# Kernel tuning notes

Hardware: AMD Instinct MI355X
Metric: run time of the kernel (lower is better)

Reference implementation:

```python
import jax, jax.numpy as jnp
import numpy as np

H, W, C, KH, KW = 16, 16, 3, 3, 3  # SOMLayer(16,16,3,3,3)
STRIDE = 2


def _extract_patches(x):
    """x: [B,C,Himg,Wimg] -> patches [B, P, C*KH*KW] in (C,kh,kw) order, P = n_out^2."""
    n_out = (x.shape[-2] - KH) // STRIDE + 1  # 15 for 32x32 input
    starts = jnp.arange(n_out) * STRIDE
    rows = starts[:, None] + jnp.arange(KH)   # [n_out, KH]
    cols = starts[:, None] + jnp.arange(KW)   # [n_out, KW]
    xr = x[:, :, rows, :]                      # [B,C,n_out,KH,Wimg]
    xrc = xr[:, :, :, :, cols]                 # [B,C,n_out,KH,n_out,KW]
    p = jnp.transpose(xrc, (0, 2, 4, 1, 3, 5)) # [B,n_out,n_out,C,KH,KW]
    return p.reshape(x.shape[0], n_out * n_out, C * KH * KW), n_out


def _som_forward(x, som):
    """Batched cdist+argmin over all windows and all 256 codebook cells.
    Faithful to the torch nested loops: winner = argmin_{m,n} mean((patch - som[m,n])^2),
    flat index m*W+n, first-occurrence tie-break (matches torch.min).
    argmin is invariant to the /27 mean scaling, so we use squared-distance GEMM form."""
    p, n_out = _extract_patches(x)             # [B,P,27]
    s = som.reshape(H * W, -1)                 # [256,27]
    d = ((p * p).sum(-1)[:, :, None]
         + (s * s).sum(-1)[None, None, :]
         - 2.0 * jnp.einsum('bpk,ck->bpc', p, s))  # [B,P,256]
    win = jnp.argmin(d, axis=-1)               # [B,P]
    m = (win // W).astype(jnp.float32) / H     # winner_r / som.shape[0]
    n = (win % W).astype(jnp.float32) / W      # winner_c / som.shape[1]
    B = x.shape[0]
    return jnp.stack([m, n], axis=1).reshape(B, 2, n_out, n_out)  # [B,2,15,15]


def setup_inputs() -> dict:
    key = jax.random.key(0)
    ks = jax.random.split(key, 10)
    B = 2048
    x = jax.random.uniform(ks[0], (B, 3, 32, 32), dtype=jnp.float32)
    # codebook (torch inits to constant 0.5 which degenerates argmin to all-ties;
    # we use a trained-like random codebook in [0,1])
    som = jax.random.uniform(ks[1], (H, W, C, KH, KW), dtype=jnp.float32)
    def lin(k, fo, fi):
        kw, kb = jax.random.split(k)
        s = 1.0 / np.sqrt(fi)
        return (jax.random.uniform(kw, (fo, fi), jnp.float32, -s, s),
                jax.random.uniform(kb, (fo,), jnp.float32, -s, s))
    W1, b1 = lin(ks[2], 400, 2 * 15 * 15)
    W2, b2 = lin(ks[3], 200, 400)
    W3, b3 = lin(ks[4], 100, 200)
    W4, b4 = lin(ks[5], 10, 100)
    return {"x": x, "som": som, "W1": W1, "b1": b1, "W2": W2, "b2": b2,
            "W3": W3, "b3": b3, "W4": W4, "b4": b4, "som_coef": 0}


def reference(x, som, W1, b1, W2, b2, W3, b3, W4, b4, som_coef):
    # som_coef=0 (and with the default momentum=1.0 the EMA update is a no-op anyway),
    # so the SOM pass is the pure winner-lookup; output is detached in torch -> stop_gradient.
    feat = jax.lax.stop_gradient(_som_forward(x, som))  # [B,2,15,15]
    h = feat.reshape(x.shape[0], -1)                    # [B,450]
    h = jax.nn.relu(h @ W1.T + b1)   # dropout in eval mode = identity
    h = jax.nn.relu(h @ W2.T + b2)
    h = jax.nn.relu(h @ W3.T + b3)
    return h @ W4.T + b4             # [B,10]
```

## Files before the change

kernel.cpp:

```cpp
#include <hip/hip_runtime.h>
#include <hip/hip_bf16.h>

#define NOUT    15
#define NPATCH  225
#define BATCH   2048
#define FEATDIM 450
#define NPTOT   (BATCH * NPATCH)
#define SOMBYTES 49152

typedef __attribute__((ext_vector_type(4))) float f32x4;
typedef __attribute__((ext_vector_type(2))) float f32x2;
typedef __attribute__((ext_vector_type(8))) short bf16x8s;

static __device__ __forceinline__ short bf2s(__hip_bfloat16 h) {
    union { __hip_bfloat16 b; short s; } u; u.b = h; return u.s;
}

__global__ void prep_som(const float* __restrict__ som, short* __restrict__ sbuf) {
    int c = threadIdx.x;
    int ct = c >> 4, col = c & 15;
    float s2 = 0.f;
    #pragma unroll
    for (int k = 0; k < 27; ++k) { float v = som[c * 27 + k]; s2 = fmaf(v, v, s2); }
    float bias = -0.5f * s2;
    #pragma unroll
    for (int kc = 0; kc < 4; ++kc)
        #pragma unroll
        for (int j = 0; j < 8; ++j) {
            int k = kc * 8 + j;
            float v = (k < 27) ? som[c * 27 + k] : ((k == 27) ? bias : 0.f);
            __hip_bfloat16 h = __float2bfloat16(v);
            float r1 = v - __bfloat162float(h);
            __hip_bfloat16 m = __float2bfloat16(r1);
            float r2 = r1 - __bfloat162float(m);
            int base = (ct * 192 + kc * 16 + col) * 8 + j;
            sbuf[base]        = bf2s(h);
            sbuf[base + 512]  = bf2s(m);
            sbuf[base + 1024] = bf2s(__float2bfloat16(r2));
        }
}

__global__ __launch_bounds__(1024, 4) void som_mfma(const float* __restrict__ x,
                                                    const short* __restrict__ sbuf,
                                                    float* __restrict__ feat) {
    __shared__ short SB[SOMBYTES / 2];

    const int tid = threadIdx.x;
    {
        const uint4* g = (const uint4*)sbuf;
        uint4* l = (uint4*)SB;
        #pragma unroll
        for (int i = 0; i < 3; ++i) l[tid + i * 1024] = g[tid + i * 1024];
    }

    const int wv   = tid >> 6;
    const int lane = tid & 63;
    const int row  = lane & 15;
    const int kc   = lane >> 4;
    const int col  = lane & 15;

    bf16x8s ah[2], am[2], al[2];
    #pragma unroll
    for (int s = 0; s < 2; ++s) {
        unsigned gp = blockIdx.x * 512u + wv * 32u + s * 16u + row;
        unsigned b  = gp / 225u;
        unsigned t  = gp - b * 225u;
        unsigned oi = t / 15u, oj = t - oi * 15u;
        const float* xb = x + (size_t)b * 3072 + oi * 64 + oj * 2;
        #pragma unroll
        for (int j = 0; j < 8; ++j) {
            int k = kc * 8 + j;
            float v = 0.f;
            if (k < 27) {
                int c = k / 9, rr = k - c * 9;
                int kh = rr / 3, kw = rr - kh * 3;
                v = xb[c * 1024 + kh * 32 + kw];
            } else if (k == 27) {
                v = 1.0f;
            }
            __hip_bfloat16 h = __float2bfloat16(v);
            float r1 = v - __bfloat162float(h);
            __hip_bfloat16 mm = __float2bfloat16(r1);
            float r2 = r1 - __bfloat162float(mm);
            ah[s][j] = bf2s(h);
            am[s][j] = bf2s(mm);
            al[s][j] = bf2s(__float2bfloat16(r2));
        }
    }
    __syncthreads();

    const bf16x8s* SBC = (const bf16x8s*)SB;

    f32x4 best[2];
    int   bidx[2][4];
    #pragma unroll
    for (int s = 0; s < 2; ++s) {
        best[s] = (f32x4){-1e30f, -1e30f, -1e30f, -1e30f};
        #pragma unroll
        for (int i = 0; i < 4; ++i) bidx[s][i] = 0;
    }

    #pragma unroll
    for (int ct = 0; ct < 16; ++ct) {
        bf16x8s bh = SBC[ct * 192 + lane];
        bf16x8s bm = SBC[ct * 192 + 64 + lane];
        bf16x8s bl = SBC[ct * 192 + 128 + lane];
        #pragma unroll
        for (int s = 0; s < 2; ++s) {
            f32x4 accA = {0.f, 0.f, 0.f, 0.f};
            f32x4 accB = {0.f, 0.f, 0.f, 0.f};
            accA = __builtin_amdgcn_mfma_f32_16x16x32_bf16(al[s], bh, accA, 0, 0, 0);
            accB = __builtin_amdgcn_mfma_f32_16x16x32_bf16(ah[s], bl, accB, 0, 0, 0);
            accA = __builtin_amdgcn_mfma_f32_16x16x32_bf16(am[s], bm, accA, 0, 0, 0);
            accB = __builtin_amdgcn_mfma_f32_16x16x32_bf16(am[s], bh, accB, 0, 0, 0);
            accA = __builtin_amdgcn_mfma_f32_16x16x32_bf16(ah[s], bm, accA, 0, 0, 0);
            accB = __builtin_amdgcn_mfma_f32_16x16x32_bf16(ah[s], bh, accB, 0, 0, 0);
            #pragma unroll
            for (int i = 0; i < 4; ++i) {
                float sc = accA[i] + accB[i];
                bool g = sc > best[s][i];
                best[s][i] = g ? sc : best[s][i];
                bidx[s][i] = g ? (ct * 16 + col) : bidx[s][i];
            }
        }
    }

    #pragma unroll
    for (int m = 1; m < 16; m <<= 1) {
        #pragma unroll
        for (int s = 0; s < 2; ++s)
            #pragma unroll
            for (int i = 0; i < 4; ++i) {
                float ob = __shfl_xor(best[s][i], m, 64);
                int   oi2 = __shfl_xor(bidx[s][i], m, 64);
                if (ob > best[s][i] || (ob == best[s][i] && oi2 < bidx[s][i])) {
                    best[s][i] = ob; bidx[s][i] = oi2;
                }
            }
    }

    if (col == 0) {
        #pragma unroll
        for (int s = 0; s < 2; ++s)
            #pragma unroll
            for (int i = 0; i < 4; ++i) {
                unsigned gp2 = blockIdx.x * 512u + wv * 32u + s * 16u + kc * 4u + i;
                unsigned b2  = gp2 / 225u;
                unsigned t2  = gp2 - b2 * 225u;
                feat[(size_t)b2 * FEATDIM + t2]          = (float)(bidx[s][i] >> 4) * 0.0625f;
                feat[(size_t)b2 * FEATDIM + NPATCH + t2] = (float)(bidx[s][i] & 15) * 0.0625f;
            }
    }
}

template <int RELU>
__global__ __launch_bounds__(128) void mlp_gemm(const float* __restrict__ A,
                                                const float* __restrict__ Wt,
                                                const float* __restrict__ bias,
                                                float* __restrict__ out,
                                                int M, int N, int K) {
    __shared__ float As[32][34];
    __shared__ float Bs[32][66];

    const int tid = threadIdx.x;
    const int m0 = blockIdx.y * 32;
    const int n0 = blockIdx.x * 64;
    const int tn = tid & 15, tm = tid >> 4;
    const int mA = tid & 31, ko = tid >> 5;
    const int nB = tid & 63, kh = tid >> 6;

    const f32x2 z2 = {0.f, 0.f};
    f32x2 pa[4], pb[8];
    float acc[4][4];
    #pragma unroll
    for (int i = 0; i < 4; ++i)
        #pragma unroll
        for (int j = 0; j < 4; ++j) acc[i][j] = 0.f;

    const bool nOk = (n0 + nB) < N;
    const int iters = (K + 31) / 32;

    #pragma unroll
    for (int q = 0; q < 4; ++q) {
        int k = ko * 8 + 2 * q;
        pa[q] = (k < K) ? *(const f32x2*)&A[(size_t)(m0 + mA) * K + k] : z2;
    }
    #pragma unroll
    for (int q = 0; q < 8; ++q) {
        int k = kh * 16 + 2 * q;
        pb[q] = (k < K && nOk) ? *(const f32x2*)&Wt[(size_t)(n0 + nB) * K + k] : z2;
    }

    for (int it = 0; it < iters; ++it) {
        #pragma unroll
        for (int q = 0; q < 4; ++q) {
            As[ko * 8 + 2 * q][mA]     = pa[q].x;
            As[ko * 8 + 2 * q + 1][mA] = pa[q].y;
        }
        #pragma unroll
        for (int q = 0; q < 8; ++q) {
            Bs[kh * 16 + 2 * q][nB]     = pb[q].x;
            Bs[kh * 16 + 2 * q + 1][nB] = pb[q].y;
        }
        __syncthreads();

        if (it + 1 < iters) {
            int kb = (it + 1) * 32;
            #pragma unroll
            for (int q = 0; q < 4; ++q) {
                int k = kb + ko * 8 + 2 * q;
                pa[q] = (k < K) ? *(const f32x2*)&A[(size_t)(m0 + mA) * K + k] : z2;
            }
            #pragma unroll
            for (int q = 0; q < 8; ++q) {
                int k = kb + kh * 16 + 2 * q;
                pb[q] = (k < K && nOk) ? *(const f32x2*)&Wt[(size_t)(n0 + nB) * K + k] : z2;
            }
        }

        #pragma unroll
        for (int k = 0; k < 32; ++k) {
            f32x4 a4 = *(const f32x4*)&As[k][tm * 4];
            f32x4 b4 = *(const f32x4*)&Bs[k][tn * 4];
            #pragma unroll
            for (int i = 0; i < 4; ++i)
                #pragma unroll
                for (int j = 0; j < 4; ++j)
                    acc[i][j] = fmaf(a4[i], b4[j], acc[i][j]);
        }
        __syncthreads();
    }

    #pragma unroll
    for (int i = 0; i < 4; ++i) {
        int m = m0 + tm * 4 + i;
        #pragma unroll
        for (int j = 0; j < 4; ++j) {
            int n = n0 + tn * 4 + j;
            if (n < N) {
                float v = acc[i][j] + bias[n];
                if (RELU) v = fmaxf(v, 0.f);
                out[(size_t)m * N + n] = v;
            }
        }
    }
}

__global__ __launch_bounds__(256) void l4_kernel(const float* __restrict__ h3,
                                                 const float* __restrict__ W4,
                                                 const float* __restrict__ b4,
                                                 float* __restrict__ out) {
    int g = blockIdx.x * 256 + threadIdx.x;
    if (g >= BATCH * 10) return;
    int m = g / 10, n = g - m * 10;
    const f32x4* a = (const f32x4*)&h3[m * 100];
    const f32x4* w = (const f32x4*)&W4[n * 100];
    float acc = 0.f;
    #pragma unroll
    for (int i = 0; i < 25; ++i) {
        f32x4 av = a[i], wv = w[i];
        acc = fmaf(av.x, wv.x, acc);
        acc = fmaf(av.y, wv.y, acc);
        acc = fmaf(av.z, wv.z, acc);
        acc = fmaf(av.w, wv.w, acc);
    }
    out[g] = acc + b4[n];
}

extern "C" void kernel_launch(void* const* d_in, const int* in_sizes, int n_in,
                              void* d_out, int out_size, void* d_ws, size_t ws_size,
                              hipStream_t stream) {
    const float* x   = (const float*)d_in[0];
    const float* som = (const float*)d_in[1];
    const float* W1  = (const float*)d_in[2];
    const float* b1  = (const float*)d_in[3];
    const float* W2  = (const float*)d_in[4];
    const float* b2  = (const float*)d_in[5];
    const float* W3  = (const float*)d_in[6];
    const float* b3  = (const float*)d_in[7];
    const float* W4  = (const float*)d_in[8];
    const float* b4  = (const float*)d_in[9];

    char* ws = (char*)d_ws;
    short* sbuf = (short*)ws;
    float* feat = (float*)(ws + SOMBYTES);
    float* h1 = feat + (size_t)BATCH * FEATDIM;
    float* h2 = h1 + (size_t)BATCH * 400;
    float* h3 = h2 + (size_t)BATCH * 200;
    float* outp = (float*)d_out;

    prep_som<<<1, 256, 0, stream>>>(som, sbuf);
    som_mfma<<<NPTOT / 512, 1024, 0, stream>>>(x, sbuf, feat);

    mlp_gemm<1><<<dim3(7, BATCH / 32), 128, 0, stream>>>(feat, W1, b1, h1, BATCH, 400, FEATDIM);
    mlp_gemm<1><<<dim3(4, BATCH / 32), 128, 0, stream>>>(h1, W2, b2, h2, BATCH, 200, 400);
    mlp_gemm<1><<<dim3(2, BATCH / 32), 128, 0, stream>>>(h2, W3, b3, h3, BATCH, 100, 200);
    l4_kernel<<<80, 256, 0, stream>>>(h3, W4, b4, outp);
}
```

Measured before the change: 217.5 us.

## Fuse MLP layers into one MFMA kernel with split-bf16 weights

Replaces the three fp32 SIMT GEMM launches and the final layer kernel with one fused kernel. Each 16-row block runs all four layers on bf16 MFMA, using three-term bf16 splits of weights and activations with bias folded in, and keeps intermediate activations in shared memory. The SOM kernel now uses 512-thread blocks, each wave handles 64 patches, and it writes bf16 features directly. A new prep kernel pre-splits the weights every call. Only 128 blocks run the MLP, so parallelism is low, and the extra prep kernel adds launch and memory work.

```diff
diff --git a/kernel.cpp b/kernel.cpp
--- a/kernel.cpp
+++ b/kernel.cpp
@@ -1,19 +1,34 @@
 #include <hip/hip_runtime.h>
-#include <hip/hip_bf16.h>
-
-#define NOUT    15
+
+#define BATCH   2048
 #define NPATCH  225
-#define BATCH   2048
-#define FEATDIM 450
 #define NPTOT   (BATCH * NPATCH)
+#define FKP     480
 #define SOMBYTES 49152
 
 typedef __attribute__((ext_vector_type(4))) float f32x4;
-typedef __attribute__((ext_vector_type(2))) float f32x2;
 typedef __attribute__((ext_vector_type(8))) short bf16x8s;
 
-static __device__ __forceinline__ short bf2s(__hip_bfloat16 h) {
-    union { __hip_bfloat16 b; short s; } u; u.b = h; return u.s;
+__device__ __forceinline__ void tsplit(float v, unsigned short& h,
+                                       unsigned short& m, unsigned short& l) {
+    unsigned bv = __float_as_uint(v);
+    h = (unsigned short)(bv >> 16);
+    float r1 = v - __uint_as_float(bv & 0xFFFF0000u);
+    unsigned br = __float_as_uint(r1);
+    m = (unsigned short)(br >> 16);
+    float r2 = r1 - __uint_as_float(br & 0xFFFF0000u);
+    l = (unsigned short)(__float_as_uint(r2) >> 16);
+}
+
+__device__ __forceinline__ f32x4 mm6(bf16x8s Ah, bf16x8s Am, bf16x8s Al,
+                                     bf16x8s Wh, bf16x8s Wm, bf16x8s Wl, f32x4 a) {
+    a = __builtin_amdgcn_mfma_f32_16x16x32_bf16(Al, Wh, a, 0, 0, 0);
+    a = __builtin_amdgcn_mfma_f32_16x16x32_bf16(Ah, Wl, a, 0, 0, 0);
+    a = __builtin_amdgcn_mfma_f32_16x16x32_bf16(Am, Wm, a, 0, 0, 0);
+    a = __builtin_amdgcn_mfma_f32_16x16x32_bf16(Am, Wh, a, 0, 0, 0);
+    a = __builtin_amdgcn_mfma_f32_16x16x32_bf16(Ah, Wm, a, 0, 0, 0);
+    a = __builtin_amdgcn_mfma_f32_16x16x32_bf16(Ah, Wh, a, 0, 0, 0);
+    return a;
 }
 
 __global__ void prep_som(const float* __restrict__ som, short* __restrict__ sbuf) {
@@ -29,28 +44,96 @@
         for (int j = 0; j < 8; ++j) {
             int k = kc * 8 + j;
             float v = (k < 27) ? som[c * 27 + k] : ((k == 27) ? bias : 0.f);
-            __hip_bfloat16 h = __float2bfloat16(v);
-            float r1 = v - __bfloat162float(h);
-            __hip_bfloat16 m = __float2bfloat16(r1);
-            float r2 = r1 - __bfloat162float(m);
+            unsigned short h, m, l;
+            tsplit(v, h, m, l);
             int base = (ct * 192 + kc * 16 + col) * 8 + j;
-            sbuf[base]        = bf2s(h);
-            sbuf[base + 512]  = bf2s(m);
-            sbuf[base + 1024] = bf2s(__float2bfloat16(r2));
-        }
-}
-
-__global__ __launch_bounds__(1024, 4) void som_mfma(const float* __restrict__ x,
-                                                    const short* __restrict__ sbuf,
-                                                    float* __restrict__ feat) {
+            sbuf[base]        = (short)h;
+            sbuf[base + 512]  = (short)m;
+            sbuf[base + 1024] = (short)l;
+        }
+}
+
+__global__ __launch_bounds__(256) void prep_w(
+        const float* __restrict__ W1, const float* __restrict__ b1,
+        const float* __restrict__ W2, const float* __restrict__ b2,
+        const float* __restrict__ W3, const float* __restrict__ b3,
+        const float* __restrict__ W4, const float* __restrict__ b4,
+        short* __restrict__ wf1, short* __restrict__ wf2,
+        short* __restrict__ wf3, short* __restrict__ wf4,
+        unsigned short* __restrict__ featbf) {
+    int id = blockIdx.x * 256 + threadIdx.x;
+    const float* W; const float* b; short* o; int N, K, tile, ch;
+    if (id < 24000) {
+        tile = id >> 6; ch = id & 63; W = W1; b = b1; N = 400; K = 450;
+        o = wf1 + (size_t)tile * 1536 + ch * 8;
+        int kc = tile % 15, nt = tile / 15;
+        int n = nt * 16 + (ch & 15), oct = ch >> 4;
+        #pragma unroll
+        for (int j = 0; j < 8; ++j) {
+            int k = kc * 32 + oct * 8 + j;
+            float v = 0.f;
+            if (n < N) { if (k < K) v = W[n * K + k]; else if (k == K) v = b[n]; }
+            unsigned short h, m, l; tsplit(v, h, m, l);
+            o[j] = (short)h; o[512 + j] = (short)m; o[1024 + j] = (short)l;
+        }
+    } else if (id < 34816) {
+        int id2 = id - 24000; tile = id2 >> 6; ch = id2 & 63; N = 200; K = 400;
+        o = wf2 + (size_t)tile * 1536 + ch * 8;
+        int kc = tile % 13, nt = tile / 13;
+        int n = nt * 16 + (ch & 15), oct = ch >> 4;
+        #pragma unroll
+        for (int j = 0; j < 8; ++j) {
+            int k = kc * 32 + oct * 8 + j;
+            float v = 0.f;
+            if (n < N) { if (k < K) v = W2[n * K + k]; else if (k == K) v = b2[n]; }
+            unsigned short h, m, l; tsplit(v, h, m, l);
+            o[j] = (short)h; o[512 + j] = (short)m; o[1024 + j] = (short)l;
+        }
+    } else if (id < 37952) {
+        int id2 = id - 34816; tile = id2 >> 6; ch = id2 & 63; N = 100; K = 200;
+        o = wf3 + (size_t)tile * 1536 + ch * 8;
+        int kc = tile % 7, nt = tile / 7;
+        int n = nt * 16 + (ch & 15), oct = ch >> 4;
+        #pragma unroll
+        for (int j = 0; j < 8; ++j) {
+            int k = kc * 32 + oct * 8 + j;
+            float v = 0.f;
+            if (n < N) { if (k < K) v = W3[n * K + k]; else if (k == K) v = b3[n]; }
+            unsigned short h, m, l; tsplit(v, h, m, l);
+            o[j] = (short)h; o[512 + j] = (short)m; o[1024 + j] = (short)l;
+        }
+    } else if (id < 38208) {
+        int id2 = id - 37952; tile = id2 >> 6; ch = id2 & 63; N = 10; K = 100;
+        o = wf4 + (size_t)tile * 1536 + ch * 8;
+        int kc = tile;
+        int n = ch & 15, oct = ch >> 4;
+        #pragma unroll
+        for (int j = 0; j < 8; ++j) {
+            int k = kc * 32 + oct * 8 + j;
+            float v = 0.f;
+            if (n < N) { if (k < K) v = W4[n * K + k]; else if (k == K) v = b4[n]; }
+            unsigned short h, m, l; tsplit(v, h, m, l);
+            o[j] = (short)h; o[512 + j] = (short)m; o[1024 + j] = (short)l;
+        }
+    } else if (id < 40256) {
+        int r = id - 38208;
+        unsigned short* f = featbf + (size_t)r * FKP + 450;
+        f[0] = 0x3F80;
+        #pragma unroll
+        for (int j = 1; j < 30; ++j) f[j] = 0;
+    }
+}
+
+__global__ __launch_bounds__(512, 4) void som_mfma(const float* __restrict__ x,
+                                                   const short* __restrict__ sbuf,
+                                                   unsigned short* __restrict__ featbf) {
     __shared__ short SB[SOMBYTES / 2];
-
     const int tid = threadIdx.x;
     {
         const uint4* g = (const uint4*)sbuf;
         uint4* l = (uint4*)SB;
         #pragma unroll
-        for (int i = 0; i < 3; ++i) l[tid + i * 1024] = g[tid + i * 1024];
+        for (int i = 0; i < 6; ++i) l[tid + i * 512] = g[tid + i * 512];
     }
 
     const int wv   = tid >> 6;
@@ -59,10 +142,10 @@
     const int kc   = lane >> 4;
     const int col  = lane & 15;
 
-    bf16x8s ah[2], am[2], al[2];
-    #pragma unroll
-    for (int s = 0; s < 2; ++s) {
-        unsigned gp = blockIdx.x * 512u + wv * 32u + s * 16u + row;
+    bf16x8s ah[4], am[4], al[4];
+    #pragma unroll
+    for (int s = 0; s < 4; ++s) {
+        unsigned gp = blockIdx.x * 512u + wv * 64u + s * 16u + row;
         unsigned b  = gp / 225u;
         unsigned t  = gp - b * 225u;
         unsigned oi = t / 15u, oj = t - oi * 15u;
@@ -78,23 +161,19 @@
             } else if (k == 27) {
                 v = 1.0f;
             }
-            __hip_bfloat16 h = __float2bfloat16(v);
-            float r1 = v - __bfloat162float(h);
-            __hip_bfloat16 mm = __float2bfloat16(r1);
-            float r2 = r1 - __bfloat162float(mm);
-            ah[s][j] = bf2s(h);
-            am[s][j] = bf2s(mm);
-            al[s][j] = bf2s(__float2bfloat16(r2));
+            unsigned short hh, mm, ll;
+            tsplit(v, hh, mm, ll);
+            ah[s][j] = (short)hh; am[s][j] = (short)mm; al[s][j] = (short)ll;
         }
     }
     __syncthreads();
 
     const bf16x8s* SBC = (const bf16x8s*)SB;
 
-    f32x4 best[2];
-    int   bidx[2][4];
-    #pragma unroll
-    for (int s = 0; s < 2; ++s) {
+    f32x4 best[4];
+    int   bidx[4][4];
+    #pragma unroll
+    for (int s = 0; s < 4; ++s) {
         best[s] = (f32x4){-1e30f, -1e30f, -1e30f, -1e30f};
         #pragma unroll
         for (int i = 0; i < 4; ++i) bidx[s][i] = 0;
@@ -106,20 +185,13 @@
         bf16x8s bm = SBC[ct * 192 + 64 + lane];
         bf16x8s bl = SBC[ct * 192 + 128 + lane];
         #pragma unroll
-        for (int s = 0; s < 2; ++s) {
-            f32x4 accA = {0.f, 0.f, 0.f, 0.f};
-            f32x4 accB = {0.f, 0.f, 0.f, 0.f};
-            accA = __builtin_amdgcn_mfma_f32_16x16x32_bf16(al[s], bh, accA, 0, 0, 0);
-            accB = __builtin_amdgcn_mfma_f32_16x16x32_bf16(ah[s], bl, accB, 0, 0, 0);
-            accA = __builtin_amdgcn_mfma_f32_16x16x32_bf16(am[s], bm, accA, 0, 0, 0);
-            accB = __builtin_amdgcn_mfma_f32_16x16x32_bf16(am[s], bh, accB, 0, 0, 0);
-            accA = __builtin_amdgcn_mfma_f32_16x16x32_bf16(ah[s], bm, accA, 0, 0, 0);
-            accB = __builtin_amdgcn_mfma_f32_16x16x32_bf16(ah[s], bh, accB, 0, 0, 0);
+        for (int s = 0; s < 4; ++s) {
+            f32x4 a = {0.f, 0.f, 0.f, 0.f};
+            a = mm6(ah[s], am[s], al[s], bh, bm, bl, a);
             #pragma unroll
             for (int i = 0; i < 4; ++i) {
-                float sc = accA[i] + accB[i];
-                bool g = sc > best[s][i];
-                best[s][i] = g ? sc : best[s][i];
+                bool g = a[i] > best[s][i];
+                best[s][i] = g ? a[i] : best[s][i];
                 bidx[s][i] = g ? (ct * 16 + col) : bidx[s][i];
             }
         }
@@ -128,7 +200,7 @@
     #pragma unroll
     for (int m = 1; m < 16; m <<= 1) {
         #pragma unroll
-        for (int s = 0; s < 2; ++s)
+        for (int s = 0; s < 4; ++s)
             #pragma unroll
             for (int i = 0; i < 4; ++i) {
                 float ob = __shfl_xor(best[s][i], m, 64);
@@ -141,130 +213,164 @@
 
     if (col == 0) {
         #pragma unroll
-        for (int s = 0; s < 2; ++s)
+        for (int s = 0; s < 4; ++s)
             #pragma unroll
             for (int i = 0; i < 4; ++i) {
-                unsigned gp2 = blockIdx.x * 512u + wv * 32u + s * 16u + kc * 4u + i;
+                unsigned gp2 = blockIdx.x * 512u + wv * 64u + s * 16u + kc * 4u + i;
                 unsigned b2  = gp2 / 225u;
                 unsigned t2  = gp2 - b2 * 225u;
-                feat[(size_t)b2 * FEATDIM + t2]          = (float)(bidx[s][i] >> 4) * 0.0625f;
-                feat[(size_t)b2 * FEATDIM + NPATCH + t2] = (float)(bidx[s][i] & 15) * 0.0625f;
-            }
-    }
-}
-
-template <int RELU>
-__global__ __launch_bounds__(128) void mlp_gemm(const float* __restrict__ A,
-                                                const float* __restrict__ Wt,
-                                                const float* __restrict__ bias,
-                                                float* __restrict__ out,
-                                                int M, int N, int K) {
-    __shared__ float As[32][34];
-    __shared__ float Bs[32][66];
-
-    const int tid = threadIdx.x;
-    const int m0 = blockIdx.y * 32;
-    const int n0 = blockIdx.x * 64;
-    const int tn = tid & 15, tm = tid >> 4;
-    const int mA = tid & 31, ko = tid >> 5;
-    const int nB = tid & 63, kh = tid >> 6;
-
-    const f32x2 z2 = {0.f, 0.f};
-    f32x2 pa[4], pb[8];
-    float acc[4][4];
-    #pragma unroll
-    for (int i = 0; i < 4; ++i)
-        #pragma unroll
-        for (int j = 0; j < 4; ++j) acc[i][j] = 0.f;
-
-    const bool nOk = (n0 + nB) < N;
-    const int iters = (K + 31) / 32;
-
-    #pragma unroll
-    for (int q = 0; q < 4; ++q) {
-        int k = ko * 8 + 2 * q;
-        pa[q] = (k < K) ? *(const f32x2*)&A[(size_t)(m0 + mA) * K + k] : z2;
-    }
-    #pragma unroll
-    for (int q = 0; q < 8; ++q) {
-        int k = kh * 16 + 2 * q;
-        pb[q] = (k < K && nOk) ? *(const f32x2*)&Wt[(size_t)(n0 + nB) * K + k] : z2;
-    }
-
-    for (int it = 0; it < iters; ++it) {
-        #pragma unroll
-        for (int q = 0; q < 4; ++q) {
-            As[ko * 8 + 2 * q][mA]     = pa[q].x;
-            As[ko * 8 + 2 * q + 1][mA] = pa[q].y;
-        }
-        #pragma unroll
-        for (int q = 0; q < 8; ++q) {
-            Bs[kh * 16 + 2 * q][nB]     = pb[q].x;
-            Bs[kh * 16 + 2 * q + 1][nB] = pb[q].y;
-        }
-        __syncthreads();
-
-        if (it + 1 < iters) {
-            int kb = (it + 1) * 32;
+                float vm = (float)(bidx[s][i] >> 4) * 0.0625f;
+                float vn = (float)(bidx[s][i] & 15) * 0.0625f;
+                featbf[(size_t)b2 * FKP + t2]       = (unsigned short)(__float_as_uint(vm) >> 16);
+                featbf[(size_t)b2 * FKP + 225 + t2] = (unsigned short)(__float_as_uint(vn) >> 16);
+            }
+    }
+}
+
+#define H1S 19968
+#define H2S 10752
+
+template <int NT, int KC, int OKC, int NVALID>
+__device__ __forceinline__ void layer_mid(const short* inS, short* outS,
+                                          const short* __restrict__ wf,
+                                          int wv, int lane) {
+    const bf16x8s* Ain = (const bf16x8s*)inS;
+    const int col = lane & 15, g = lane >> 4;
+    constexpr int TPW = (NT + 7) / 8;
+    f32x4 acc[TPW];
+    #pragma unroll
+    for (int i = 0; i < TPW; ++i) acc[i] = (f32x4){0.f, 0.f, 0.f, 0.f};
+    #pragma unroll
+    for (int kc = 0; kc < KC; ++kc) {
+        bf16x8s Ah = Ain[(0 * KC + kc) * 64 + lane];
+        bf16x8s Am = Ain[(1 * KC + kc) * 64 + lane];
+        bf16x8s Al = Ain[(2 * KC + kc) * 64 + lane];
+        #pragma unroll
+        for (int ti = 0; ti < TPW; ++ti) {
+            int t = wv + ti * 8;
+            if (t < NT) {
+                const bf16x8s* W = (const bf16x8s*)(wf + (size_t)(t * KC + kc) * 1536);
+                acc[ti] = mm6(Ah, Am, Al, W[lane], W[64 + lane], W[128 + lane], acc[ti]);
+            }
+        }
+    }
+    #pragma unroll
+    for (int ti = 0; ti < TPW; ++ti) {
+        int t = wv + ti * 8;
+        if (t < NT) {
+            int k = t * 16 + col;
+            if (k < NVALID) {
+                int kc2 = k >> 5, oct = (k >> 3) & 3, j = k & 7;
+                #pragma unroll
+                for (int i = 0; i < 4; ++i) {
+                    int r = g * 4 + i;
+                    float v = fmaxf(acc[ti][i], 0.f);
+                    unsigned short hh, mm, ll;
+                    tsplit(v, hh, mm, ll);
+                    outS[((0 * OKC + kc2) * 64 + oct * 16 + r) * 8 + j] = (short)hh;
+                    outS[((1 * OKC + kc2) * 64 + oct * 16 + r) * 8 + j] = (short)mm;
+                    outS[((2 * OKC + kc2) * 64 + oct * 16 + r) * 8 + j] = (short)ll;
+                }
+            }
+        }
+    }
+}
+
+template <int OKC, int K0, int NS>
+__device__ __forceinline__ void pad_init(short* outS, int tid) {
+    for (int p = tid; p < NS * 16 * 3; p += 512) {
+        int term = p / (NS * 16);
+        int rem  = p % (NS * 16);
+        int ks   = K0 + rem / 16;
+        int r    = rem % 16;
+        unsigned short v = (ks == K0 && term == 0) ? 0x3F80 : 0;
+        outS[((term * OKC + (ks >> 5)) * 64 + ((ks >> 3) & 3) * 16 + r) * 8 + (ks & 7)] = (short)v;
+    }
+}
+
+__global__ __launch_bounds__(512) void fused_mlp(
+        const unsigned short* __restrict__ featbf,
+        const short* __restrict__ wf1, const short* __restrict__ wf2,
+        const short* __restrict__ wf3, const short* __restrict__ wf4,
+        float* __restrict__ out) {
+    __shared__ short FB[H1S + H2S];
+
+    const int tid  = threadIdx.x;
+    const int wv   = tid >> 6;
+    const int lane = tid & 63;
+    const int col  = lane & 15, g = lane >> 4;
+    const int blk  = blockIdx.x;
+
+    const unsigned short* fb = featbf + (size_t)(blk * 16 + col) * FKP;
+    bf16x8s af[15];
+    #pragma unroll
+    for (int kc = 0; kc < 15; ++kc)
+        af[kc] = *(const bf16x8s*)(fb + kc * 32 + g * 8);
+
+    f32x4 acc1[4];
+    #pragma unroll
+    for (int i = 0; i < 4; ++i) acc1[i] = (f32x4){0.f, 0.f, 0.f, 0.f};
+    #pragma unroll
+    for (int kc = 0; kc < 15; ++kc) {
+        #pragma unroll
+        for (int ti = 0; ti < 4; ++ti) {
+            int t = wv + ti * 8;
+            if (t < 25) {
+                const bf16x8s* W = (const bf16x8s*)(wf1 + (size_t)(t * 15 + kc) * 1536);
+                f32x4 a = acc1[ti];
+                a = __builtin_amdgcn_mfma_f32_16x16x32_bf16(af[kc], W[128 + lane], a, 0, 0, 0);
+                a = __builtin_amdgcn_mfma_f32_16x16x32_bf16(af[kc], W[64 + lane],  a, 0, 0, 0);
+                a = __builtin_amdgcn_mfma_f32_16x16x32_bf16(af[kc], W[lane],       a, 0, 0, 0);
+                acc1[ti] = a;
+            }
+        }
+    }
+    #pragma unroll
+    for (int ti = 0; ti < 4; ++ti) {
+        int t = wv + ti * 8;
+        if (t < 25) {
+            int k = t * 16 + col;
+            int kc2 = k >> 5, oct = (k >> 3) & 3, j = k & 7;
             #pragma unroll
-            for (int q = 0; q < 4; ++q) {
-                int k = kb + ko * 8 + 2 * q;
-                pa[q] = (k < K) ? *(const f32x2*)&A[(size_t)(m0 + mA) * K + k] : z2;
-            }
-            #pragma unroll
-            for (int q = 0; q < 8; ++q) {
-                int k = kb + kh * 16 + 2 * q;
-                pb[q] = (k < K && nOk) ? *(const f32x2*)&Wt[(size_t)(n0 + nB) * K + k] : z2;
-            }
-        }
-
-        #pragma unroll
-        for (int k = 0; k < 32; ++k) {
-            f32x4 a4 = *(const f32x4*)&As[k][tm * 4];
-            f32x4 b4 = *(const f32x4*)&Bs[k][tn * 4];
+            for (int i = 0; i < 4; ++i) {
+                int r = g * 4 + i;
+                float v = fmaxf(acc1[ti][i], 0.f);
+                unsigned short hh, mm, ll;
+                tsplit(v, hh, mm, ll);
+                FB[((0 * 13 + kc2) * 64 + oct * 16 + r) * 8 + j] = (short)hh;
+                FB[((1 * 13 + kc2) * 64 + oct * 16 + r) * 8 + j] = (short)mm;
+                FB[((2 * 13 + kc2) * 64 + oct * 16 + r) * 8 + j] = (short)ll;
+            }
+        }
+    }
+    pad_init<13, 400, 16>(FB, tid);
+    __syncthreads();
+
+    layer_mid<13, 13, 7, 200>(FB, FB + H1S, wf2, wv, lane);
+    pad_init<7, 200, 24>(FB + H1S, tid);
+    __syncthreads();
+
+    layer_mid<7, 7, 4, 100>(FB + H1S, FB, wf3, wv, lane);
+    pad_init<4, 100, 28>(FB, tid);
+    __syncthreads();
+
+    if (wv == 0) {
+        const bf16x8s* Ain = (const bf16x8s*)FB;
+        f32x4 a = {0.f, 0.f, 0.f, 0.f};
+        #pragma unroll
+        for (int kc = 0; kc < 4; ++kc) {
+            bf16x8s Ah = Ain[(0 * 4 + kc) * 64 + lane];
+            bf16x8s Am = Ain[(1 * 4 + kc) * 64 + lane];
+            bf16x8s Al = Ain[(2 * 4 + kc) * 64 + lane];
+            const bf16x8s* W = (const bf16x8s*)(wf4 + (size_t)kc * 1536);
+            a = mm6(Ah, Am, Al, W[lane], W[64 + lane], W[128 + lane], a);
+        }
+        if (col < 10) {
             #pragma unroll
             for (int i = 0; i < 4; ++i)
-                #pragma unroll
-                for (int j = 0; j < 4; ++j)
-                    acc[i][j] = fmaf(a4[i], b4[j], acc[i][j]);
-        }
-        __syncthreads();
-    }
-
-    #pragma unroll
-    for (int i = 0; i < 4; ++i) {
-        int m = m0 + tm * 4 + i;
-        #pragma unroll
-        for (int j = 0; j < 4; ++j) {
-            int n = n0 + tn * 4 + j;
-            if (n < N) {
-                float v = acc[i][j] + bias[n];
-                if (RELU) v = fmaxf(v, 0.f);
-                out[(size_t)m * N + n] = v;
-            }
-        }
-    }
-}
-
-__global__ __launch_bounds__(256) void l4_kernel(const float* __restrict__ h3,
-                                                 const float* __restrict__ W4,
-                                                 const float* __restrict__ b4,
-                                                 float* __restrict__ out) {
-    int g = blockIdx.x * 256 + threadIdx.x;
-    if (g >= BATCH * 10) return;
-    int m = g / 10, n = g - m * 10;
-    const f32x4* a = (const f32x4*)&h3[m * 100];
-    const f32x4* w = (const f32x4*)&W4[n * 100];
-    float acc = 0.f;
-    #pragma unroll
-    for (int i = 0; i < 25; ++i) {
-        f32x4 av = a[i], wv = w[i];
-        acc = fmaf(av.x, wv.x, acc);
-        acc = fmaf(av.y, wv.y, acc);
-        acc = fmaf(av.z, wv.z, acc);
-        acc = fmaf(av.w, wv.w, acc);
-    }
-    out[g] = acc + b4[n];
+                out[(size_t)(blk * 16 + g * 4 + i) * 10 + col] = a[i];
+        }
+    }
 }
 
 extern "C" void kernel_launch(void* const* d_in, const int* in_sizes, int n_in,
@@ -282,18 +388,17 @@
     const float* b4  = (const float*)d_in[9];
 
     char* ws = (char*)d_ws;
-    short* sbuf = (short*)ws;
-    float* feat = (float*)(ws + SOMBYTES);
-    float* h1 = feat + (size_t)BATCH * FEATDIM;
-    float* h2 = h1 + (size_t)BATCH * 400;
-    float* h3 = h2 + (size_t)BATCH * 200;
+    short*          sbuf   = (short*)ws;
+    unsigned short* featbf = (unsigned short*)(ws + 49152);
+    short*          wf1    = (short*)(ws + 2015232);
+    short*          wf2    = (short*)(ws + 3167232);
+    short*          wf3    = (short*)(ws + 3686400);
+    short*          wf4    = (short*)(ws + 3836928);
     float* outp = (float*)d_out;
 
     prep_som<<<1, 256, 0, stream>>>(som, sbuf);
-    som_mfma<<<NPTOT / 512, 1024, 0, stream>>>(x, sbuf, feat);
-
-    mlp_gemm<1><<<dim3(7, BATCH / 32), 128, 0, stream>>>(feat, W1, b1, h1, BATCH, 400, FEATDIM);
-    mlp_gemm<1><<<dim3(4, BATCH / 32), 128, 0, stream>>>(h1, W2, b2, h2, BATCH, 200, 400);
-    mlp_gemm<1><<<dim3(2, BATCH / 32), 128, 0, stream>>>(h2, W3, b3, h3, BATCH, 100, 200);
-    l4_kernel<<<80, 256, 0, stream>>>(h3, W4, b4, outp);
-}
+    prep_w<<<158, 256, 0, stream>>>(W1, b1, W2, b2, W3, b3, W4, b4,
+                                    wf1, wf2, wf3, wf4, featbf);
+    som_mfma<<<900, 512, 0, stream>>>(x, sbuf, featbf);
+    fused_mlp<<<128, 512, 0, stream>>>(featbf, wf1, wf2, wf3, wf4, outp);
+}
```

Result: faster. 195.3 us (-10.2%).
